# Kernel tuning notes

Measured on AMD Instinct MI355X. Metric: run time of the kernel, lower is better.

The kernel has to match this reference:

```python
import math
import jax, jax.numpy as jnp
import numpy as np

B, T, HIDDEN = 2, 2048, 1024
H, HKV, D = 16, 16, 64


def _rope_tables(T, D):
    inv_freq = 1.0 / (10000.0 ** (jnp.arange(0, D, 2, dtype=jnp.float32) / D))
    t = jnp.arange(T, dtype=jnp.float32)
    freqs = jnp.outer(t, inv_freq)               # [T, D/2]
    emb = jnp.concatenate([freqs, freqs], axis=-1)  # [T, D]
    return jnp.cos(emb), jnp.sin(emb)


def setup_inputs() -> dict:
    key = jax.random.key(0)
    k1, k2, k3 = jax.random.split(key, 3)
    hidden_states = jax.random.normal(k1, (B, T, HIDDEN), dtype=jnp.float32)
    cos, sin = _rope_tables(T, D)
    # trunc-normal-ish init, std = 1/sqrt(fan_in)
    w_qkv = jax.random.normal(k2, ((H + 2 * HKV) * D, HIDDEN), dtype=jnp.float32) / math.sqrt(HIDDEN)
    w_o = jax.random.normal(k3, (HIDDEN, H * D), dtype=jnp.float32) / math.sqrt(H * D)
    return {"hidden_states": hidden_states, "cos": cos, "sin": sin, "w_qkv": w_qkv, "w_o": w_o}


def _rotate_half(x):
    x1, x2 = jnp.split(x, 2, axis=-1)
    return jnp.concatenate([-x2, x1], axis=-1)


def reference(hidden_states, cos, sin, w_qkv, w_o):
    b, t, _ = hidden_states.shape
    # fused QKV projection: [B,T,(H+2*HKV)*D]
    qkv = jnp.einsum('bti,oi->bto', hidden_states, w_qkv)
    qkv = qkv.reshape(b, t, H + 2 * HKV, D)
    q = qkv[:, :, :H]                    # [B,T,H,D]
    k = qkv[:, :, H:H + HKV]             # [B,T,HKV,D]
    v = qkv[:, :, H + HKV:]              # [B,T,HKV,D]
    # inline RoPE; cos/sin broadcast over heads
    c = cos[:, None, :]
    s = sin[:, None, :]
    q = q * c + _rotate_half(q) * s
    k = k * c + _rotate_half(k) * s
    scale = 1.0 / math.sqrt(D)
    attn_scores = jnp.einsum('bthd,bThd->bhtT', q, k) * scale  # [B,H,T,T]
    mask = jnp.tril(jnp.ones((t, t), dtype=bool))
    attn_scores = jnp.where(mask[None, None, :, :], attn_scores, -1e9)
    attn = jax.nn.softmax(attn_scores, axis=-1)
    context = jnp.einsum('bhtT,bThd->bthd', attn, v).reshape(b, t, H * D)
    return jnp.einsum('bti,oi->bto', context, w_o)
```

## Files before the change

kernel.cpp:

```cpp
#include <hip/hip_runtime.h>

typedef __bf16 bf16_t;
typedef __bf16 bf16x4 __attribute__((ext_vector_type(4)));
typedef __bf16 bf16x8 __attribute__((ext_vector_type(8)));
typedef float f32x4 __attribute__((ext_vector_type(4)));
typedef unsigned int u32x2 __attribute__((ext_vector_type(2)));
typedef unsigned long long u64;

#define MFMA16(a, b, c) __builtin_amdgcn_mfma_f32_16x16x32_bf16((a), (b), (c), 0, 0, 0)

#define LDG2LDS16(g, l)                                                        \
    __builtin_amdgcn_global_load_lds(                                          \
        (const __attribute__((address_space(1))) void*)(g),                    \
        (__attribute__((address_space(3))) void*)(l), 16, 0, 0)

#if __has_builtin(__builtin_amdgcn_exp2f)
#define EXP2(x) __builtin_amdgcn_exp2f(x)
#else
#define EXP2(x) exp2f(x)
#endif

__device__ inline bf16x8 load8(const float* p) {
    const f32x4 a = *(const f32x4*)p;
    const f32x4 b = *(const f32x4*)(p + 4);
    bf16x8 r;
#pragma unroll
    for (int i = 0; i < 4; i++) { r[i] = (bf16_t)a[i]; r[4 + i] = (bf16_t)b[i]; }
    return r;
}

__device__ inline u32x2 as2(bf16x4 v) {
    u32x2 r;
    __builtin_memcpy(&r, &v, 8);
    return r;
}

__device__ inline bf16x4 shfl4(bf16x4 v, int src) {
    u64 x;
    __builtin_memcpy(&x, &v, 8);
    x = __shfl(x, src, 64);
    bf16x4 r;
    __builtin_memcpy(&r, &x, 8);
    return r;
}

__global__ __launch_bounds__(256) void convert_kernel(const float* __restrict__ hs,
                                                      const float* __restrict__ wqkv,
                                                      const float* __restrict__ wo,
                                                      bf16_t* __restrict__ outb) {
    const size_t c = ((size_t)blockIdx.x * 256 + threadIdx.x) * 8;
    const float* src;
    size_t off;
    if (c < 4194304) { src = hs; off = c; }
    else if (c < 7340032) { src = wqkv; off = c - 4194304; }
    else { src = wo; off = c - 7340032; }
    *(bf16x8*)(outb + c) = load8(src + off);
}


template <int MODE, int NDIM, int BM>
__global__ __launch_bounds__(256) void gemm_bt(const bf16_t* __restrict__ A,
                                               const bf16_t* __restrict__ B,
                                               float* __restrict__ outp,
                                               bf16_t* __restrict__ q_ws,
                                               bf16_t* __restrict__ k_ws,
                                               bf16_t* __restrict__ v_ws,
                                               const float* __restrict__ cosb,
                                               const float* __restrict__ sinb) {
    constexpr int K = 1024;
    constexpr int IM = BM / 32;
    __shared__ __align__(16) bf16_t As[BM * 32];
    __shared__ __align__(16) bf16_t Bs[128 * 32];

    const int tid = threadIdx.x;
    const int w = tid >> 6;
    const int lane = tid & 63;
    const int lr = lane & 15;
    const int quad = lane >> 4;
    const int m0 = blockIdx.y * BM;
    const int n0 = blockIdx.x * 128;
    const int wm = (w & 1) * (BM / 2);
    const int wn = (w >> 1) * 64;

    const int srow = tid >> 2;
    const int skk = (tid & 3) * 8;
    const bf16_t* gA0 = A + (size_t)(m0 + srow) * K + skk;
    const bf16_t* gA1 = gA0 + (size_t)64 * K;
    const bf16_t* gB0 = B + (size_t)(n0 + srow) * K + skk;
    const bf16_t* gB1 = gB0 + (size_t)64 * K;
    bf16_t* lA0 = As + w * 512;
    bf16_t* lA1 = As + 2048 + w * 512;
    bf16_t* lB0 = Bs + w * 512;
    bf16_t* lB1 = Bs + 2048 + w * 512;

    f32x4 acc[IM][4] = {};

    for (int k0 = 0; k0 < K; k0 += 32) {
        LDG2LDS16(gA0 + k0, lA0);
        if constexpr (BM == 128) LDG2LDS16(gA1 + k0, lA1);
        LDG2LDS16(gB0 + k0, lB0);
        LDG2LDS16(gB1 + k0, lB1);
        __syncthreads();

        bf16x8 af[IM], bfm[4];
#pragma unroll
        for (int im = 0; im < IM; im++)
            af[im] = *(const bf16x8*)&As[(wm + im * 16 + lr) * 32 + quad * 8];
#pragma unroll
        for (int in = 0; in < 4; in++)
            bfm[in] = *(const bf16x8*)&Bs[(wn + in * 16 + lr) * 32 + quad * 8];
#pragma unroll
        for (int im = 0; im < IM; im++)
#pragma unroll
            for (int in = 0; in < 4; in++)
                acc[im][in] = MFMA16(af[im], bfm[in], acc[im][in]);
        __syncthreads();
    }

    if constexpr (MODE == 0) {
#pragma unroll
        for (int im = 0; im < IM; im++)
#pragma unroll
            for (int in = 0; in < 4; in++)
#pragma unroll
                for (int r = 0; r < 4; r++) {
                    const int m = m0 + wm + im * 16 + quad * 4 + r;
                    const int n = n0 + wn + in * 16 + lr;
                    outp[(size_t)m * NDIM + n] = acc[im][in][r];
                }
    } else {
        const int j = (n0 + wn) >> 6;
        if (j < 32) {
            const bool isq = (j < 16);
            const float qs = 0.125f * 1.44269504089f;
#pragma unroll
            for (int im = 0; im < IM; im++) {
#pragma unroll
                for (int r = 0; r < 4; r++) {
                    const int m = m0 + wm + im * 16 + quad * 4 + r;
                    const int b = m >> 11;
                    const int t = m & 2047;
#pragma unroll
                    for (int in = 0; in < 2; in++) {
                        const int d = in * 16 + lr;
                        const float x1 = acc[im][in][r];
                        const float x2 = acc[im][in + 2][r];
                        const float c = cosb[t * 64 + d];
                        const float s = sinb[t * 64 + d];
                        float y1 = x1 * c - x2 * s;
                        float y2 = x2 * c + x1 * s;
                        if (isq) {
                            y1 *= qs; y2 *= qs;
                            const size_t base =
                                ((size_t)(b * 16 + j) * 2048 + t) * 64 + d;
                            q_ws[base] = (bf16_t)y1;
                            q_ws[base + 32] = (bf16_t)y2;
                        } else {
                            const int bh = b * 16 + (j - 16);
                            const size_t off =
                                ((size_t)(bh * 128 + (t >> 4)) * 2) * 512 +
                                ((t & 15) + (d >> 3) * 16) * 8 + (d & 7);
                            k_ws[off] = (bf16_t)y1;
                            k_ws[off + 512] = (bf16_t)y2;
                        }
                    }
                }
            }
        } else {
#pragma unroll
            for (int im = 0; im < IM; im++)
#pragma unroll
                for (int in = 0; in < 4; in++)
#pragma unroll
                    for (int r = 0; r < 4; r++) {
                        const int m = m0 + wm + im * 16 + quad * 4 + r;
                        const int b = m >> 11;
                        const int t = m & 2047;
                        const int d = in * 16 + lr;
                        const int bh = b * 16 + (j - 32);
                        const size_t off =
                            ((size_t)(bh * 64 + (t >> 5)) * 4 + (d >> 4)) * 512 +
                            ((d & 15) + ((t & 31) >> 3) * 16) * 8 + (t & 7);
                        v_ws[off] = (bf16_t)acc[im][in][r];
                    }
        }
    }
}

__device__ inline void flash_tile(int qt, int quad, int lr, int query,
                                  const bf16_t* __restrict__ kbase,
                                  const bf16_t* __restrict__ vbase,
                                  bf16x8 qlo, bf16x8 qhi,
                                  f32x4* o, float& lrun) {
    bf16x8 kc[8];
#pragma unroll
    for (int n = 0; n < 4; n++) {
        kc[2 * n] = *(const bf16x8*)(kbase + (size_t)(n * 2) * 512);
        kc[2 * n + 1] = *(const bf16x8*)(kbase + (size_t)(n * 2 + 1) * 512);
    }

    for (int kb = 0; kb <= qt; kb++) {
        bf16x8 vv[2][4];
#pragma unroll
        for (int hh = 0; hh < 2; hh++)
#pragma unroll
            for (int n = 0; n < 4; n++)
                vv[hh][n] = *(const bf16x8*)(vbase +
                    (size_t)((kb * 2 + hh) * 4 + n) * 512);

        const int kbn = (kb < qt) ? kb + 1 : kb;
        bf16x8 kn[8];
#pragma unroll
        for (int n = 0; n < 4; n++) {
            kn[2 * n] = *(const bf16x8*)(kbase + (size_t)((kbn * 4 + n) * 2) * 512);
            kn[2 * n + 1] = *(const bf16x8*)(kbase + (size_t)((kbn * 4 + n) * 2 + 1) * 512);
        }

        const int u0 = kb * 64;
        f32x4 s[4];
#pragma unroll
        for (int n = 0; n < 4; n++) {
            const f32x4 z = {};
            s[n] = MFMA16(kc[2 * n], qlo, z);
            s[n] = MFMA16(kc[2 * n + 1], qhi, s[n]);
        }

        if (kb == qt) {
#pragma unroll
            for (int n = 0; n < 4; n++)
#pragma unroll
                for (int r = 0; r < 4; r++)
                    if (u0 + n * 16 + quad * 4 + r > query) s[n][r] = -1e9f;
        }

        f32x4 p[4];
#pragma unroll
        for (int n = 0; n < 4; n++)
#pragma unroll
            for (int r = 0; r < 4; r++) p[n][r] = EXP2(s[n][r]);

        lrun += ((p[0][0] + p[0][1]) + (p[0][2] + p[0][3])) +
                ((p[1][0] + p[1][1]) + (p[1][2] + p[1][3])) +
                ((p[2][0] + p[2][1]) + (p[2][2] + p[2][3])) +
                ((p[3][0] + p[3][1]) + (p[3][2] + p[3][3]));

        bf16x4 pb[4];
#pragma unroll
        for (int n = 0; n < 4; n++)
#pragma unroll
            for (int r = 0; r < 4; r++) pb[n][r] = (bf16_t)p[n][r];

#pragma unroll
        for (int hh = 0; hh < 2; hh++) {
            bf16x8 pf;
#if __has_builtin(__builtin_amdgcn_permlane16_swap) && \
    __has_builtin(__builtin_amdgcn_permlane32_swap)
            const u32x2 P0 = as2(pb[2 * hh]);
            const u32x2 P1 = as2(pb[2 * hh + 1]);
            const u32x2 s1a = __builtin_amdgcn_permlane16_swap(P0[0], P0[1], false, false);
            const u32x2 s1b = __builtin_amdgcn_permlane16_swap(P1[0], P1[1], false, false);
            const u32x2 s2a = __builtin_amdgcn_permlane32_swap(s1a[0], s1b[0], false, false);
            const u32x2 s2b = __builtin_amdgcn_permlane32_swap(s1a[1], s1b[1], false, false);
            const u32x2 s3a = __builtin_amdgcn_permlane16_swap(s2a[0], s2a[1], false, false);
            const u32x2 s3b = __builtin_amdgcn_permlane16_swap(s2b[0], s2b[1], false, false);
            const unsigned pfd[4] = {s3a[0], s3a[1], s3b[0], s3b[1]};
            __builtin_memcpy(&pf, pfd, 16);
#else
            const int srcLow = ((quad & 1) << 5) + lr;
            const int srcHigh = srcLow + 16;
            const bool loSel = (quad < 2);
            const bf16x4 a0 = shfl4(pb[2 * hh], srcLow);
            const bf16x4 a1 = shfl4(pb[2 * hh + 1], srcLow);
            const bf16x4 b0 = shfl4(pb[2 * hh], srcHigh);
            const bf16x4 b1 = shfl4(pb[2 * hh + 1], srcHigh);
            const bf16x4 lo = loSel ? a0 : a1;
            const bf16x4 hi = loSel ? b0 : b1;
#pragma unroll
            for (int r = 0; r < 4; r++) { pf[r] = lo[r]; pf[4 + r] = hi[r]; }
#endif
#pragma unroll
            for (int n = 0; n < 4; n++)
                o[n] = MFMA16(vv[hh][n], pf, o[n]);
        }

#pragma unroll
        for (int i = 0; i < 8; i++) kc[i] = kn[i];
    }
}

__global__ __launch_bounds__(256) void attn_kernel(const bf16_t* __restrict__ q_ws,
                                                   const bf16_t* __restrict__ k_ws,
                                                   const bf16_t* __restrict__ v_ws,
                                                   bf16_t* __restrict__ ctx) {
    const int tid = threadIdx.x;
    const int w = tid >> 6;
    const int lane = tid & 63;
    const int lr = lane & 15;
    const int quad = lane >> 4;
    const int bh = blockIdx.x & 31;
    const int pr = blockIdx.x >> 5;
    const int b = bh >> 4;
    const int hd = bh & 15;

    const bf16_t* kbase = k_ws + (size_t)bh * 131072 + lane * 8;
    const bf16_t* vbase = v_ws + (size_t)bh * 131072 + lane * 8;

#pragma unroll
    for (int half = 0; half < 2; half++) {
        const int qt = half ? (31 - pr) : pr;
        const int trow = qt * 64 + w * 16;
        const int query = trow + lr;

        const bf16_t* qb = q_ws + ((size_t)bh * 2048 + trow + lr) * 64 + quad * 8;
        const bf16x8 qlo = *(const bf16x8*)qb;
        const bf16x8 qhi = *(const bf16x8*)(qb + 32);

        f32x4 o[4] = {};
        float lrun = 0.0f;
        flash_tile(qt, quad, lr, query, kbase, vbase, qlo, qhi, o, lrun);

        lrun += __shfl_xor(lrun, 16);
        lrun += __shfl_xor(lrun, 32);

        const float inv = 1.0f / fmaxf(lrun, 1e-30f);
        const size_t base = ((size_t)b * 2048 + query) * 1024 + hd * 64 + quad * 4;
#pragma unroll
        for (int n = 0; n < 4; n++) {
            bf16x4 ob;
#pragma unroll
            for (int r = 0; r < 4; r++) ob[r] = (bf16_t)(o[n][r] * inv);
            *(bf16x4*)&ctx[base + n * 16] = ob;
        }
    }
}

extern "C" void kernel_launch(void* const* d_in, const int* in_sizes, int n_in,
                              void* d_out, int out_size, void* d_ws, size_t ws_size,
                              hipStream_t stream) {
    const float* hs = (const float*)d_in[0];
    const float* cosb = (const float*)d_in[1];
    const float* sinb = (const float*)d_in[2];
    const float* wqkv = (const float*)d_in[3];
    const float* wo = (const float*)d_in[4];
    float* out = (float*)d_out;

    char* ws = (char*)d_ws;
    bf16_t* hs_b = (bf16_t*)(ws);
    bf16_t* wqkv_b = hs_b + 4194304;
    bf16_t* wo_b = hs_b + 7340032;
    bf16_t* q_ws = (bf16_t*)(ws + (size_t)(16u << 20));
    bf16_t* k_ws = (bf16_t*)(ws + (size_t)(24u << 20));
    bf16_t* v_ws = (bf16_t*)(ws + (size_t)(32u << 20));
    bf16_t* ctx = (bf16_t*)(ws);

    const dim3 blk(256);

    convert_kernel<<<dim3(4096), blk, 0, stream>>>(hs, wqkv, wo, hs_b);

    gemm_bt<1, 3072, 128><<<dim3(24, 32), blk, 0, stream>>>(
        hs_b, wqkv_b, nullptr, q_ws, k_ws, v_ws, cosb, sinb);

    attn_kernel<<<dim3(512), blk, 0, stream>>>(q_ws, k_ws, v_ws, ctx);

    gemm_bt<0, 1024, 64><<<dim3(8, 64), blk, 0, stream>>>(
        ctx, wo_b, out, nullptr, nullptr, nullptr, nullptr, nullptr);
}
```

Before: 178.4 us.

## Replace QKV GEMM with 256x256-tile, 512-thread, double-buffered kernel

Adds a dedicated QKV projection kernel that uses 256x256 output tiles with 8 waves. K-tiles of 64 are staged into double-buffered swizzled LDS through direct global-to-LDS loads, and block IDs are remapped for locality. MFMA issue is wrapped in raised wave priority. RoPE, the Q scaling and the K/V layout writes are fused into the epilogue. The larger tile increases operand reuse and cuts global traffic, but it launches only 192 blocks, so some CUs may sit idle. It also holds 128 accumulator registers per thread.

```diff
diff --git a/kernel.cpp b/kernel.cpp
--- a/kernel.cpp
+++ b/kernel.cpp
@@ -57,6 +57,173 @@
     *(bf16x8*)(outb + c) = load8(src + off);
 }
 
+
+__global__ __launch_bounds__(512, 2) void gemm_qkv256(const bf16_t* __restrict__ A,
+                                                      const bf16_t* __restrict__ B,
+                                                      bf16_t* __restrict__ q_ws,
+                                                      bf16_t* __restrict__ k_ws,
+                                                      bf16_t* __restrict__ v_ws,
+                                                      const float* __restrict__ cosb,
+                                                      const float* __restrict__ sinb) {
+    constexpr int K = 1024;
+    __shared__ __align__(16) bf16_t As[32768];
+    __shared__ __align__(16) bf16_t Bs[32768];
+
+    const int tid = threadIdx.x;
+    const int w = tid >> 6;
+    const int lane = tid & 63;
+    const int lr = lane & 15;
+    const int quad = lane >> 4;
+
+    const int lid = blockIdx.x;
+    const int l = (lid & 7) * 24 + (lid >> 3);
+    const int by = l / 12;
+    const int bx = l - by * 12;
+    const int m0 = by * 256;
+    const int n0 = bx * 256;
+
+    const int trow = tid >> 3;
+    const int slot = (tid & 7) ^ (trow & 7);
+    const bf16_t* gA = A + (size_t)(m0 + trow) * K + slot * 8;
+    const bf16_t* gB = B + (size_t)(n0 + trow) * K + slot * 8;
+    bf16_t* lA = As + w * 512;
+    bf16_t* lB = Bs + w * 512;
+
+    const int wmm = (w >> 2) * 128;
+    const int wnn = (w & 3) * 64;
+    const int offA0 = (quad ^ (lr & 7)) * 16;
+    const char* Ab = (const char*)As + (wmm + lr) * 128;
+    const char* Bb = (const char*)Bs + (wnn + lr) * 128;
+
+    f32x4 acc[8][4] = {};
+
+#define STAGE256(t, buf)                                                       \
+    {                                                                          \
+        _Pragma("unroll") for (int c = 0; c < 4; c++) {                        \
+            LDG2LDS16(gA + (size_t)c * 65536 + (size_t)(t) * 64,               \
+                      lA + (buf) * 16384 + c * 4096);                          \
+            LDG2LDS16(gB + (size_t)c * 65536 + (size_t)(t) * 64,               \
+                      lB + (buf) * 16384 + c * 4096);                          \
+        }                                                                      \
+    }
+
+#define PHASE256(buf, qm, qn)                                                  \
+    {                                                                          \
+        const char* pa = Ab + (buf) * 32768 + (qm) * 8192;                     \
+        const char* pb = Bb + (buf) * 32768 + (qn) * 4096;                     \
+        {                                                                      \
+            bf16x8 a0[4], b0[2];                                               \
+            _Pragma("unroll") for (int i = 0; i < 4; i++)                      \
+                a0[i] = *(const bf16x8*)(pa + i * 2048 + offA0);               \
+            _Pragma("unroll") for (int jn = 0; jn < 2; jn++)                   \
+                b0[jn] = *(const bf16x8*)(pb + jn * 2048 + offA0);             \
+            __builtin_amdgcn_s_setprio(1);                                     \
+            _Pragma("unroll") for (int i = 0; i < 4; i++)                      \
+                _Pragma("unroll") for (int jn = 0; jn < 2; jn++)               \
+                    acc[(qm) * 4 + i][(qn) * 2 + jn] = MFMA16(                 \
+                        a0[i], b0[jn], acc[(qm) * 4 + i][(qn) * 2 + jn]);      \
+            __builtin_amdgcn_s_setprio(0);                                     \
+        }                                                                      \
+        {                                                                      \
+            bf16x8 a1[4], b1[2];                                               \
+            _Pragma("unroll") for (int i = 0; i < 4; i++)                      \
+                a1[i] = *(const bf16x8*)(pa + i * 2048 + (offA0 ^ 64));        \
+            _Pragma("unroll") for (int jn = 0; jn < 2; jn++)                   \
+                b1[jn] = *(const bf16x8*)(pb + jn * 2048 + (offA0 ^ 64));      \
+            __builtin_amdgcn_s_setprio(1);                                     \
+            _Pragma("unroll") for (int i = 0; i < 4; i++)                      \
+                _Pragma("unroll") for (int jn = 0; jn < 2; jn++)               \
+                    acc[(qm) * 4 + i][(qn) * 2 + jn] = MFMA16(                 \
+                        a1[i], b1[jn], acc[(qm) * 4 + i][(qn) * 2 + jn]);      \
+            __builtin_amdgcn_s_setprio(0);                                     \
+        }                                                                      \
+    }
+
+    STAGE256(0, 0);
+    STAGE256(1, 1);
+    asm volatile("s_waitcnt vmcnt(8)" ::: "memory");
+    __builtin_amdgcn_s_barrier();
+    asm volatile("" ::: "memory");
+
+#pragma unroll 2
+    for (int t = 0; t < 16; t++) {
+        const int buf = t & 1;
+        PHASE256(buf, 0, 0);
+        PHASE256(buf, 0, 1);
+        PHASE256(buf, 1, 0);
+        PHASE256(buf, 1, 1);
+        asm volatile("s_waitcnt lgkmcnt(0)" ::: "memory");
+        __builtin_amdgcn_s_barrier();
+        asm volatile("" ::: "memory");
+        if (t < 14) {
+            STAGE256(t + 2, buf);
+            asm volatile("s_waitcnt vmcnt(8)" ::: "memory");
+        } else {
+            asm volatile("s_waitcnt vmcnt(0)" ::: "memory");
+        }
+        __builtin_amdgcn_s_barrier();
+        asm volatile("" ::: "memory");
+    }
+
+#undef STAGE256
+#undef PHASE256
+
+    const int j = bx * 4 + (w & 3);
+    if (j < 32) {
+        const bool isq = (j < 16);
+        const float qs = 0.125f * 1.44269504089f;
+#pragma unroll
+        for (int im = 0; im < 8; im++) {
+#pragma unroll
+            for (int r = 0; r < 4; r++) {
+                const int m = m0 + wmm + im * 16 + quad * 4 + r;
+                const int b = m >> 11;
+                const int t = m & 2047;
+#pragma unroll
+                for (int in = 0; in < 2; in++) {
+                    const int d = in * 16 + lr;
+                    const float x1 = acc[im][in][r];
+                    const float x2 = acc[im][in + 2][r];
+                    const float c = cosb[t * 64 + d];
+                    const float s = sinb[t * 64 + d];
+                    float y1 = x1 * c - x2 * s;
+                    float y2 = x2 * c + x1 * s;
+                    if (isq) {
+                        y1 *= qs; y2 *= qs;
+                        const size_t base =
+                            ((size_t)(b * 16 + j) * 2048 + t) * 64 + d;
+                        q_ws[base] = (bf16_t)y1;
+                        q_ws[base + 32] = (bf16_t)y2;
+                    } else {
+                        const int bh = b * 16 + (j - 16);
+                        const size_t off =
+                            ((size_t)(bh * 128 + (t >> 4)) * 2) * 512 +
+                            ((t & 15) + (d >> 3) * 16) * 8 + (d & 7);
+                        k_ws[off] = (bf16_t)y1;
+                        k_ws[off + 512] = (bf16_t)y2;
+                    }
+                }
+            }
+        }
+    } else {
+#pragma unroll
+        for (int im = 0; im < 8; im++)
+#pragma unroll
+            for (int in = 0; in < 4; in++)
+#pragma unroll
+                for (int r = 0; r < 4; r++) {
+                    const int m = m0 + wmm + im * 16 + quad * 4 + r;
+                    const int b = m >> 11;
+                    const int t = m & 2047;
+                    const int d = in * 16 + lr;
+                    const int bh = b * 16 + (j - 32);
+                    const size_t off =
+                        ((size_t)(bh * 64 + (t >> 5)) * 4 + (d >> 4)) * 512 +
+                        ((d & 15) + ((t & 31) >> 3) * 16) * 8 + (t & 7);
+                    v_ws[off] = (bf16_t)acc[im][in][r];
+                }
+    }
+}
 
 template <int MODE, int NDIM, int BM>
 __global__ __launch_bounds__(256) void gemm_bt(const bf16_t* __restrict__ A,
@@ -357,8 +524,8 @@
 
     convert_kernel<<<dim3(4096), blk, 0, stream>>>(hs, wqkv, wo, hs_b);
 
-    gemm_bt<1, 3072, 128><<<dim3(24, 32), blk, 0, stream>>>(
-        hs_b, wqkv_b, nullptr, q_ws, k_ws, v_ws, cosb, sinb);
+    gemm_qkv256<<<dim3(192), dim3(512), 0, stream>>>(
+        hs_b, wqkv_b, q_ws, k_ws, v_ws, cosb, sinb);
 
     attn_kernel<<<dim3(512), blk, 0, stream>>>(q_ws, k_ws, v_ws, ctx);
 
```

Measured after the change: 189.0 us. 1.06x slower.

## Double GEMM K-tile to 64 with XOR-swizzled LDS layout

Applied to the files above, without the earlier changes.

The projection GEMM now stages 64-wide K slices per iteration, so it runs 16 iterations instead of 32 and halves the number of block barriers. The LDS rows are stored with an XOR swizzle on the 16-byte slot index, which is meant to avoid bank conflicts when the MFMA fragments are read. LDS use doubles per block, which may lower occupancy.

```diff
diff --git a/kernel.cpp b/kernel.cpp
--- a/kernel.cpp
+++ b/kernel.cpp
@@ -69,8 +69,8 @@
                                                const float* __restrict__ sinb) {
     constexpr int K = 1024;
     constexpr int IM = BM / 32;
-    __shared__ __align__(16) bf16_t As[BM * 32];
-    __shared__ __align__(16) bf16_t Bs[128 * 32];
+    __shared__ __align__(16) bf16_t As[BM * 64];
+    __shared__ __align__(16) bf16_t Bs[128 * 64];
 
     const int tid = threadIdx.x;
     const int w = tid >> 6;
@@ -82,38 +82,44 @@
     const int wm = (w & 1) * (BM / 2);
     const int wn = (w >> 1) * 64;
 
-    const int srow = tid >> 2;
-    const int skk = (tid & 3) * 8;
-    const bf16_t* gA0 = A + (size_t)(m0 + srow) * K + skk;
-    const bf16_t* gA1 = gA0 + (size_t)64 * K;
-    const bf16_t* gB0 = B + (size_t)(n0 + srow) * K + skk;
-    const bf16_t* gB1 = gB0 + (size_t)64 * K;
-    bf16_t* lA0 = As + w * 512;
-    bf16_t* lA1 = As + 2048 + w * 512;
-    bf16_t* lB0 = Bs + w * 512;
-    bf16_t* lB1 = Bs + 2048 + w * 512;
+    const int trow = tid >> 3;
+    const int slot = (tid & 7) ^ (trow & 7);
+    const bf16_t* gA = A + (size_t)(m0 + trow) * K + slot * 8;
+    const bf16_t* gB = B + (size_t)(n0 + trow) * K + slot * 8;
+    bf16_t* lA = As + w * 512;
+    bf16_t* lB = Bs + w * 512;
+
+    const int o0 = (quad ^ (lr & 7)) * 16;
+    const char* Ab = (const char*)As + (wm + lr) * 128;
+    const char* Bb = (const char*)Bs + (wn + lr) * 128;
 
     f32x4 acc[IM][4] = {};
 
-    for (int k0 = 0; k0 < K; k0 += 32) {
-        LDG2LDS16(gA0 + k0, lA0);
-        if constexpr (BM == 128) LDG2LDS16(gA1 + k0, lA1);
-        LDG2LDS16(gB0 + k0, lB0);
-        LDG2LDS16(gB1 + k0, lB1);
+    for (int t = 0; t < 16; t++) {
+#pragma unroll
+        for (int c = 0; c < BM / 32; c++)
+            LDG2LDS16(gA + (size_t)c * 32 * K + t * 64, lA + c * 2048);
+#pragma unroll
+        for (int c = 0; c < 4; c++)
+            LDG2LDS16(gB + (size_t)c * 32 * K + t * 64, lB + c * 2048);
         __syncthreads();
 
-        bf16x8 af[IM], bfm[4];
-#pragma unroll
-        for (int im = 0; im < IM; im++)
-            af[im] = *(const bf16x8*)&As[(wm + im * 16 + lr) * 32 + quad * 8];
-#pragma unroll
-        for (int in = 0; in < 4; in++)
-            bfm[in] = *(const bf16x8*)&Bs[(wn + in * 16 + lr) * 32 + quad * 8];
-#pragma unroll
-        for (int im = 0; im < IM; im++)
+#pragma unroll
+        for (int kh = 0; kh < 2; kh++) {
+            const int so = o0 ^ (kh * 64);
+            bf16x8 af[IM], bfm[4];
+#pragma unroll
+            for (int im = 0; im < IM; im++)
+                af[im] = *(const bf16x8*)(Ab + im * 2048 + so);
 #pragma unroll
             for (int in = 0; in < 4; in++)
-                acc[im][in] = MFMA16(af[im], bfm[in], acc[im][in]);
+                bfm[in] = *(const bf16x8*)(Bb + in * 2048 + so);
+#pragma unroll
+            for (int im = 0; im < IM; im++)
+#pragma unroll
+                for (int in = 0; in < 4; in++)
+                    acc[im][in] = MFMA16(af[im], bfm[in], acc[im][in]);
+        }
         __syncthreads();
     }
 
```

Result: slower. 189.8 us (+6.4%).
